# Kernel optimization log

Measured on AMD Instinct MI355X. Metric: run time of the kernel, lower is better.

The kernel has to match this reference:

```python
import jax, jax.numpy as jnp
import numpy as np

N_NODES = 50000
N_EDGES = 800000
IN_FEAT = 128
HIDDEN = 256
NUM_LAYERS = 4
NUM_CLASSES = 10
NUM_GRAPHS = 128
BN_EPS = 1e-5


def setup_inputs() -> dict:
    key = jax.random.key(0)
    ks = jax.random.split(key, 8)
    x = jax.random.normal(ks[0], (N_NODES, IN_FEAT), dtype=jnp.float32)
    edge_index = jax.random.randint(ks[1], (2, N_EDGES), 0, N_NODES, dtype=jnp.int64)
    batch = jax.random.randint(ks[2], (N_NODES,), 0, NUM_GRAPHS, dtype=jnp.int64)
    W1 = jax.random.normal(ks[3], (IN_FEAT, HIDDEN), dtype=jnp.float32) * 0.05
    b1 = jnp.zeros((HIDDEN,), jnp.float32)
    gamma = jnp.ones((HIDDEN,), jnp.float32)
    beta = jnp.zeros((HIDDEN,), jnp.float32)
    run_mean = jnp.zeros((HIDDEN,), jnp.float32)
    run_var = jnp.ones((HIDDEN,), jnp.float32)
    Ws = jax.random.normal(ks[4], (NUM_LAYERS - 1, HIDDEN, HIDDEN), dtype=jnp.float32) * 0.05
    bs = jnp.zeros((NUM_LAYERS - 1, HIDDEN), jnp.float32)
    W2 = jax.random.normal(ks[5], (HIDDEN, NUM_CLASSES), dtype=jnp.float32) * 0.05
    b2 = jnp.zeros((NUM_CLASSES,), jnp.float32)
    return {"x": x, "edge_index": edge_index, "batch": batch,
            "W1": W1, "b1": b1, "gamma": gamma, "beta": beta,
            "run_mean": run_mean, "run_var": run_var,
            "Ws": Ws, "bs": bs, "W2": W2, "b2": b2}


def _gcn_conv(h, W, b, src, dst, norm, n):
    # x' = D^-1/2 (A+I) D^-1/2 (x W) + b   (PyG GCNConv with self-loops)
    h = h @ W                                   # [N, out]
    msg = h[src] * norm[:, None]                # [E+N, out]
    agg = jax.ops.segment_sum(msg, dst, num_segments=n)
    return agg + b


def reference(x, edge_index, batch, W1, b1, gamma, beta, run_mean, run_var, Ws, bs, W2, b2):
    n = x.shape[0]
    loop = jnp.arange(n, dtype=edge_index.dtype)
    src = jnp.concatenate([edge_index[0], loop])
    dst = jnp.concatenate([edge_index[1], loop])
    # symmetric GCN normalization with self-loops (deg >= 1, no inf)
    deg = jax.ops.segment_sum(jnp.ones_like(dst, x.dtype), dst, num_segments=n)
    dinv = jax.lax.rsqrt(deg)
    norm = dinv[src] * dinv[dst]

    h = _gcn_conv(x, W1, b1, src, dst, norm, n)
    # BatchNorm in eval mode: running statistics
    h = (h - run_mean) * jax.lax.rsqrt(run_var + BN_EPS) * gamma + beta
    h = jax.nn.relu(h)
    for i in range(Ws.shape[0]):
        h = jax.nn.relu(_gcn_conv(h, Ws[i], bs[i], src, dst, norm, n))

    # global mean pool over graphs
    sums = jax.ops.segment_sum(h, batch, num_segments=NUM_GRAPHS)
    cnts = jax.ops.segment_sum(jnp.ones((n,), x.dtype), batch, num_segments=NUM_GRAPHS)
    pooled = sums / jnp.maximum(cnts, 1.0)[:, None]

    logits = pooled @ W2 + b2
    return jax.nn.log_softmax(logits, axis=-1)
```

## Files before the change

kernel.cpp:

```cpp
#include <hip/hip_runtime.h>
#include <math.h>

#define N_NODES 50000
#define N_EDGES 800000
#define IN_FEAT 128
#define HIDDEN 256
#define NUM_GRAPHS 128
#define NUM_CLASSES 10
#define BN_EPS 1e-5f

#define NCHUNK ((N_NODES + 255) / 256)
#define BINW 512
#define NBINS ((N_NODES + BINW - 1) / BINW)

typedef __attribute__((ext_vector_type(8))) short bf16x8;
typedef __attribute__((ext_vector_type(16))) float f32x16;
typedef __attribute__((ext_vector_type(2))) float f32x2;

__device__ __forceinline__ ushort f2bf(float f) {
    union { float f; uint u; } c; c.f = f;
    uint u = c.u;
    return (ushort)((u + 0x7FFFu + ((u >> 16) & 1u)) >> 16);
}
__device__ __forceinline__ float bf2f(ushort h) {
    union { uint u; float f; } c; c.u = ((uint)h) << 16;
    return c.f;
}
__device__ __forceinline__ unsigned char f2fp8(float f) {
    return (unsigned char)(__builtin_amdgcn_cvt_pk_fp8_f32(f, f, 0, false) & 0xFF);
}

__global__ void k_count(const int* __restrict__ dst, int* __restrict__ cnt) {
    int e = blockIdx.x * 256 + threadIdx.x;
    if (e < N_EDGES) atomicAdd(&cnt[dst[e]], 1);
}

__global__ __launch_bounds__(512) void k_count_batch(const int* __restrict__ batch,
                                                     int* __restrict__ gcnt) {
    __shared__ int hist[NUM_GRAPHS];
    int t = threadIdx.x;
    if (t < NUM_GRAPHS) hist[t] = 0;
    __syncthreads();
    int v = blockIdx.x * 512 + t;
    if (v < N_NODES) atomicAdd(&hist[batch[v]], 1);
    __syncthreads();
    if (t < NUM_GRAPHS && hist[t] > 0) atomicAdd(&gcnt[t], hist[t]);
}

__global__ __launch_bounds__(256) void k_chunksum(const int* __restrict__ cnt,
                                                  int* __restrict__ csum) {
    int i = blockIdx.x * 256 + threadIdx.x;
    int v = (i < N_NODES) ? cnt[i] : 0;
#pragma unroll
    for (int off = 32; off; off >>= 1) v += __shfl_down(v, off, 64);
    __shared__ int ws[4];
    if ((threadIdx.x & 63) == 0) ws[threadIdx.x >> 6] = v;
    __syncthreads();
    if (threadIdx.x == 0) csum[blockIdx.x] = ws[0] + ws[1] + ws[2] + ws[3];
}

__global__ __launch_bounds__(256) void k_scan2(const int* __restrict__ csum,
                                               int* __restrict__ choff,
                                               const int* __restrict__ gcnt,
                                               int* __restrict__ goff,
                                               int* __restrict__ gcur) {
    __shared__ int s[256];
    int t = threadIdx.x;
    if (blockIdx.x == 0) {
        int v = (t < NCHUNK) ? csum[t] : 0;
        s[t] = v;
        __syncthreads();
#pragma unroll
        for (int off = 1; off < 256; off <<= 1) {
            int add = (t >= off) ? s[t - off] : 0;
            __syncthreads();
            s[t] += add;
            __syncthreads();
        }
        if (t < NCHUNK) choff[t] = s[t] - v;
    } else {
        int v = (t < NUM_GRAPHS) ? gcnt[t] : 0;
        s[t] = v;
        __syncthreads();
#pragma unroll
        for (int off = 1; off < NUM_GRAPHS; off <<= 1) {
            int add = (t >= off && t < NUM_GRAPHS) ? s[t - off] : 0;
            __syncthreads();
            if (t < NUM_GRAPHS) s[t] += add;
            __syncthreads();
        }
        if (t < NUM_GRAPHS) {
            goff[t] = s[t] - v;
            gcur[t] = s[t] - v;
            if (t == NUM_GRAPHS - 1) goff[NUM_GRAPHS] = s[t];
        }
    }
}

__global__ __launch_bounds__(256) void k_apply(const int* __restrict__ cnt,
                                               const int* __restrict__ choff,
                                               int* __restrict__ rowp,
                                               float* __restrict__ dinv) {
    __shared__ int s[256];
    int t = threadIdx.x;
    int i = blockIdx.x * 256 + t;
    int c = (i < N_NODES) ? cnt[i] : 0;
    s[t] = c;
    __syncthreads();
#pragma unroll
    for (int off = 1; off < 256; off <<= 1) {
        int add = (t >= off) ? s[t - off] : 0;
        __syncthreads();
        s[t] += add;
        __syncthreads();
    }
    int incl = s[t];
    int base = choff[blockIdx.x];
    if (i < N_NODES) {
        int ex = base + incl - c;
        rowp[i] = ex;
        dinv[i] = rsqrtf(1.0f + (float)c);
        if (i == N_NODES - 1) rowp[N_NODES] = base + incl;
    }
}

__global__ void k_initbins(const int* __restrict__ rowp, int* __restrict__ bincur) {
    int b = threadIdx.x;
    if (b < NBINS) bincur[b] = rowp[b * BINW];
}

#define FILLA_EPT 8
__global__ __launch_bounds__(256) void k_binA(const int* __restrict__ src,
                                              const int* __restrict__ dst,
                                              int* __restrict__ bincur,
                                              uint* __restrict__ pairs) {
    __shared__ int hist[NBINS];
    __shared__ int base[NBINS];
    int t = threadIdx.x;
    for (int i = t; i < NBINS; i += 256) hist[i] = 0;
    __syncthreads();
    int e0 = blockIdx.x * (256 * FILLA_EPT);
    int mybin[FILLA_EPT], myoff[FILLA_EPT];
    uint mypair[FILLA_EPT];
#pragma unroll
    for (int j = 0; j < FILLA_EPT; ++j) {
        int e = e0 + j * 256 + t;
        mybin[j] = -1;
        if (e < N_EDGES) {
            int d = dst[e], s = src[e];
            int b = d >> 9;
            mybin[j] = b;
            mypair[j] = (uint)s | ((uint)(d & (BINW - 1)) << 16);
            myoff[j] = atomicAdd(&hist[b], 1);
        }
    }
    __syncthreads();
    for (int i = t; i < NBINS; i += 256)
        base[i] = atomicAdd(&bincur[i], hist[i]);
    __syncthreads();
#pragma unroll
    for (int j = 0; j < FILLA_EPT; ++j) {
        if (mybin[j] >= 0) pairs[base[mybin[j]] + myoff[j]] = mypair[j];
    }
}

__global__ __launch_bounds__(512) void k_binB(const uint* __restrict__ pairs,
                                              const int* __restrict__ rowp,
                                              int* __restrict__ col) {
    __shared__ int cur[BINW];
    int b = blockIdx.x;
    int v0 = b * BINW;
    int t = threadIdx.x;
    int vend = min(v0 + BINW, N_NODES);
    for (int i = t; i < vend - v0; i += 512) cur[i] = rowp[v0 + i];
    __syncthreads();
    int lo = rowp[v0];
    int hi = rowp[vend];
    for (int i = lo + t; i < hi; i += 512) {
        uint pr = pairs[i];
        int dl = pr >> 16;
        int s = pr & 0xFFFF;
        int slot = atomicAdd(&cur[dl], 1);
        col[slot] = s;
    }
}

__global__ __launch_bounds__(512) void k_fillg(const int* __restrict__ batch,
                                               int* __restrict__ gcur,
                                               int* __restrict__ nlist) {
    __shared__ int hist[NUM_GRAPHS];
    __shared__ int base[NUM_GRAPHS];
    int t = threadIdx.x;
    if (t < NUM_GRAPHS) hist[t] = 0;
    __syncthreads();
    int v = blockIdx.x * 512 + t;
    int g = -1, off = 0;
    if (v < N_NODES) {
        g = batch[v];
        off = atomicAdd(&hist[g], 1);
    }
    __syncthreads();
    if (t < NUM_GRAPHS) base[t] = atomicAdd(&gcur[t], hist[t]);
    __syncthreads();
    if (g >= 0) nlist[base[g] + off] = v;
}

__global__ void k_prescale(const float* __restrict__ x, const float* __restrict__ dinv,
                           unsigned char* __restrict__ p0) {
    int i = blockIdx.x * 256 + threadIdx.x;
    if (i < N_NODES * IN_FEAT / 4) {
        float4 v = ((const float4*)x)[i];
        float d = dinv[i / (IN_FEAT / 4)];
        uchar4 o;
        o.x = f2fp8(v.x * d); o.y = f2fp8(v.y * d);
        o.z = f2fp8(v.z * d); o.w = f2fp8(v.w * d);
        ((uchar4*)p0)[i] = o;
    }
}

__global__ __launch_bounds__(256) void k_agg128(const unsigned char* __restrict__ p,
                                                const int* __restrict__ col,
                                                const int* __restrict__ row_ptr,
                                                const float* __restrict__ dinv,
                                                ushort* __restrict__ out) {
    const int F = IN_FEAT;
    int wave = threadIdx.x >> 6;
    int lane = threadIdx.x & 63;
    int v = blockIdx.x * 4 + wave;
    if (v >= N_NODES) return;
    int rp0 = row_ptr[v], rp1 = row_ptr[v + 1];
    float d = dinv[v];
    ushort um = ((const ushort*)(p + (size_t)v * F))[lane];
    f32x2 m = __builtin_amdgcn_cvt_pk_f32_fp8((int)um, false);
    float a0 = m.x, a1 = m.y;
    int i = rp0;
    for (; i + 8 <= rp1; i += 8) {
        int s0 = col[i],     s1 = col[i + 1], s2 = col[i + 2], s3 = col[i + 3];
        int s4 = col[i + 4], s5 = col[i + 5], s6 = col[i + 6], s7 = col[i + 7];
        ushort u0 = ((const ushort*)(p + (size_t)s0 * F))[lane];
        ushort u1 = ((const ushort*)(p + (size_t)s1 * F))[lane];
        ushort u2 = ((const ushort*)(p + (size_t)s2 * F))[lane];
        ushort u3 = ((const ushort*)(p + (size_t)s3 * F))[lane];
        ushort u4 = ((const ushort*)(p + (size_t)s4 * F))[lane];
        ushort u5 = ((const ushort*)(p + (size_t)s5 * F))[lane];
        ushort u6 = ((const ushort*)(p + (size_t)s6 * F))[lane];
        ushort u7 = ((const ushort*)(p + (size_t)s7 * F))[lane];
        f32x2 d0 = __builtin_amdgcn_cvt_pk_f32_fp8((int)u0, false);
        f32x2 d1 = __builtin_amdgcn_cvt_pk_f32_fp8((int)u1, false);
        f32x2 d2 = __builtin_amdgcn_cvt_pk_f32_fp8((int)u2, false);
        f32x2 d3 = __builtin_amdgcn_cvt_pk_f32_fp8((int)u3, false);
        f32x2 d4 = __builtin_amdgcn_cvt_pk_f32_fp8((int)u4, false);
        f32x2 d5 = __builtin_amdgcn_cvt_pk_f32_fp8((int)u5, false);
        f32x2 d6 = __builtin_amdgcn_cvt_pk_f32_fp8((int)u6, false);
        f32x2 d7 = __builtin_amdgcn_cvt_pk_f32_fp8((int)u7, false);
        a0 += d0.x + d1.x + d2.x + d3.x + d4.x + d5.x + d6.x + d7.x;
        a1 += d0.y + d1.y + d2.y + d3.y + d4.y + d5.y + d6.y + d7.y;
    }
    for (; i < rp1; ++i) {
        int s = col[i];
        ushort u = ((const ushort*)(p + (size_t)s * F))[lane];
        f32x2 dv = __builtin_amdgcn_cvt_pk_f32_fp8((int)u, false);
        a0 += dv.x; a1 += dv.y;
    }
    ushort2 o;
    o.x = f2bf(a0 * d); o.y = f2bf(a1 * d);
    ((ushort2*)(out + (size_t)v * F))[lane] = o;
}

__global__ __launch_bounds__(256) void k_agg8(const unsigned char* __restrict__ p,
                                              const int* __restrict__ col,
                                              const int* __restrict__ row_ptr,
                                              const float* __restrict__ dinv,
                                              ushort* __restrict__ out) {
    const int F = HIDDEN;
    int wave = threadIdx.x >> 6;
    int lane = threadIdx.x & 63;
    int v = blockIdx.x * 4 + wave;
    if (v >= N_NODES) return;
    int rp0 = row_ptr[v], rp1 = row_ptr[v + 1];
    float d = dinv[v];
    uint um = ((const uint*)(p + (size_t)v * F))[lane];
    f32x2 mlo = __builtin_amdgcn_cvt_pk_f32_fp8((int)um, false);
    f32x2 mhi = __builtin_amdgcn_cvt_pk_f32_fp8((int)um, true);
    float a0 = mlo.x, a1 = mlo.y, a2 = mhi.x, a3 = mhi.y;
    int i = rp0;
    for (; i + 8 <= rp1; i += 8) {
        int s0 = col[i],     s1 = col[i + 1], s2 = col[i + 2], s3 = col[i + 3];
        int s4 = col[i + 4], s5 = col[i + 5], s6 = col[i + 6], s7 = col[i + 7];
        uint u0 = ((const uint*)(p + (size_t)s0 * F))[lane];
        uint u1 = ((const uint*)(p + (size_t)s1 * F))[lane];
        uint u2 = ((const uint*)(p + (size_t)s2 * F))[lane];
        uint u3 = ((const uint*)(p + (size_t)s3 * F))[lane];
        uint u4 = ((const uint*)(p + (size_t)s4 * F))[lane];
        uint u5 = ((const uint*)(p + (size_t)s5 * F))[lane];
        uint u6 = ((const uint*)(p + (size_t)s6 * F))[lane];
        uint u7 = ((const uint*)(p + (size_t)s7 * F))[lane];
#pragma unroll
        for (int j = 0; j < 8; ++j) {
            uint u = (j == 0) ? u0 : (j == 1) ? u1 : (j == 2) ? u2 : (j == 3) ? u3
                   : (j == 4) ? u4 : (j == 5) ? u5 : (j == 6) ? u6 : u7;
            f32x2 lo = __builtin_amdgcn_cvt_pk_f32_fp8((int)u, false);
            f32x2 hi = __builtin_amdgcn_cvt_pk_f32_fp8((int)u, true);
            a0 += lo.x; a1 += lo.y; a2 += hi.x; a3 += hi.y;
        }
    }
    for (; i < rp1; ++i) {
        int s = col[i];
        uint u = ((const uint*)(p + (size_t)s * F))[lane];
        f32x2 lo = __builtin_amdgcn_cvt_pk_f32_fp8((int)u, false);
        f32x2 hi = __builtin_amdgcn_cvt_pk_f32_fp8((int)u, true);
        a0 += lo.x; a1 += lo.y; a2 += hi.x; a3 += hi.y;
    }
    ushort4 o;
    o.x = f2bf(a0 * d); o.y = f2bf(a1 * d); o.z = f2bf(a2 * d); o.w = f2bf(a3 * d);
    ((ushort4*)(out + (size_t)v * F))[lane] = o;
}

__device__ __forceinline__ void repack_one(const float* W, ushort* Wp, int KT, int tid) {
    int lane = tid & 63;
    int kt = (tid >> 6) % KT;
    int nt = (tid >> 6) / KT;
    int n = nt * 32 + (lane & 31);
    int kb = kt * 16 + (lane >> 5) * 8;
    ushort o[8];
#pragma unroll
    for (int j = 0; j < 8; ++j) o[j] = f2bf(W[(size_t)(kb + j) * HIDDEN + n]);
    ushort4* dst = (ushort4*)(Wp + (size_t)tid * 8);
    dst[0] = make_ushort4(o[0], o[1], o[2], o[3]);
    dst[1] = make_ushort4(o[4], o[5], o[6], o[7]);
}

__global__ __launch_bounds__(256) void k_repackAll(const float* __restrict__ W1,
                                                   const float* __restrict__ Wsp,
                                                   ushort* __restrict__ Wp1,
                                                   ushort* __restrict__ Wp2,
                                                   ushort* __restrict__ Wp3,
                                                   ushort* __restrict__ Wp4) {
    const int N1 = 8 * 8 * 64;
    const int NH = 8 * 16 * 64;
    int tid = blockIdx.x * 256 + threadIdx.x;
    if (tid < N1) repack_one(W1, Wp1, 8, tid);
    else if (tid < N1 + NH) repack_one(Wsp + 0 * HIDDEN * HIDDEN, Wp2, 16, tid - N1);
    else if (tid < N1 + 2 * NH) repack_one(Wsp + 1 * HIDDEN * HIDDEN, Wp3, 16, tid - N1 - NH);
    else if (tid < N1 + 3 * NH) repack_one(Wsp + 2 * HIDDEN * HIDDEN, Wp4, 16, tid - N1 - 2 * NH);
}

template <int KDIM, int EPI>
__global__ __launch_bounds__(256) void k_mgemm(const ushort* __restrict__ A,
                                               const ushort* __restrict__ Wp,
                                               const float* __restrict__ bias,
                                               const float* __restrict__ gamma,
                                               const float* __restrict__ beta,
                                               const float* __restrict__ mean,
                                               const float* __restrict__ var,
                                               const float* __restrict__ dinv,
                                               unsigned char* __restrict__ out) {
    constexpr int KT = KDIM / 16;
    int t = threadIdx.x;
    int wv = t >> 6, lane = t & 63;
    int rg = wv >> 1;
    int ch = wv & 1;
    int row0 = blockIdx.x * 64 + rg * 32;
    int nt0 = ch * 4;
    int r32 = lane & 31, hh = lane >> 5;
    int arow = row0 + r32;
    if (arow >= N_NODES) arow = N_NODES - 1;

    f32x16 acc[4];
#pragma unroll
    for (int j = 0; j < 4; ++j)
#pragma unroll
        for (int r = 0; r < 16; ++r) acc[j][r] = 0.f;

    const ushort* aptr = A + (size_t)arow * KDIM + hh * 8;
#pragma unroll
    for (int kt = 0; kt < KT; ++kt) {
        bf16x8 af = *(const bf16x8*)(aptr + kt * 16);
#pragma unroll
        for (int j = 0; j < 4; ++j) {
            bf16x8 bfv = *(const bf16x8*)(Wp + ((size_t)((nt0 + j) * KT + kt) * 64 + lane) * 8);
            acc[j] = __builtin_amdgcn_mfma_f32_32x32x16_bf16(af, bfv, acc[j], 0, 0, 0);
        }
    }

    int rowb = row0 + 4 * hh;
    float bi[4], sc[4], sh[4];
#pragma unroll
    for (int j = 0; j < 4; ++j) {
        int colc = (nt0 + j) * 32 + r32;
        bi[j] = bias[colc];
        if constexpr (EPI == 0) {
            float s = gamma[colc] * rsqrtf(var[colc] + BN_EPS);
            sc[j] = s; sh[j] = beta[colc] - mean[colc] * s;
        }
    }
#pragma unroll
    for (int r = 0; r < 16; ++r) {
        int grow = rowb + (r & 3) + 8 * (r >> 2);
        if (grow < N_NODES) {
            float d = (EPI == 2) ? 1.f : dinv[grow];
#pragma unroll
            for (int j = 0; j < 4; ++j) {
                float y = acc[j][r] + bi[j];
                if constexpr (EPI == 0) y = y * sc[j] + sh[j];
                y = fmaxf(y, 0.f);
                y *= d;
                out[(size_t)grow * HIDDEN + (nt0 + j) * 32 + r32] = f2fp8(y);
            }
        }
    }
}

__global__ __launch_bounds__(256) void k_pool2(const unsigned char* __restrict__ h,
                                               const int* __restrict__ nlist,
                                               const int* __restrict__ goff,
                                               float* __restrict__ sums) {
    int bid = blockIdx.x;
    int chunk = bid & 3;
    int half = (bid >> 2) & 1;
    int g = bid >> 3;
    int lo = goff[g], hi = goff[g + 1];
    int w = threadIdx.x >> 6, l = threadIdx.x & 63;
    const unsigned char* hp = h + half * 128 + l * 2;
    float a0 = 0.f, a1 = 0.f;
    int i = lo + chunk * 4 + w;
    for (; i + 48 < hi; i += 64) {
        int v0 = nlist[i], v1 = nlist[i + 16], v2 = nlist[i + 32], v3 = nlist[i + 48];
        uchar2 q0 = *(const uchar2*)(hp + (size_t)v0 * HIDDEN);
        uchar2 q1 = *(const uchar2*)(hp + (size_t)v1 * HIDDEN);
        uchar2 q2 = *(const uchar2*)(hp + (size_t)v2 * HIDDEN);
        uchar2 q3 = *(const uchar2*)(hp + (size_t)v3 * HIDDEN);
        f32x2 d0 = __builtin_amdgcn_cvt_pk_f32_fp8((int)(q0.x | (q0.y << 8)), false);
        f32x2 d1 = __builtin_amdgcn_cvt_pk_f32_fp8((int)(q1.x | (q1.y << 8)), false);
        f32x2 d2 = __builtin_amdgcn_cvt_pk_f32_fp8((int)(q2.x | (q2.y << 8)), false);
        f32x2 d3 = __builtin_amdgcn_cvt_pk_f32_fp8((int)(q3.x | (q3.y << 8)), false);
        a0 += d0.x + d1.x + d2.x + d3.x;
        a1 += d0.y + d1.y + d2.y + d3.y;
    }
    for (; i < hi; i += 16) {
        int v = nlist[i];
        uchar2 q = *(const uchar2*)(hp + (size_t)v * HIDDEN);
        f32x2 dv = __builtin_amdgcn_cvt_pk_f32_fp8((int)(q.x | (q.y << 8)), false);
        a0 += dv.x; a1 += dv.y;
    }
    __shared__ float red[4][128];
    red[w][l * 2] = a0;
    red[w][l * 2 + 1] = a1;
    __syncthreads();
    int t = threadIdx.x;
    if (t < 128) {
        float s = red[0][t] + red[1][t] + red[2][t] + red[3][t];
        atomicAdd(&sums[(size_t)g * HIDDEN + half * 128 + t], s);
    }
}

__global__ __launch_bounds__(256) void k_logits(const float* __restrict__ sums,
                                                const int* __restrict__ gcnt,
                                                const float* __restrict__ W2,
                                                const float* __restrict__ b2,
                                                float* __restrict__ outp) {
    __shared__ float pooled[HIDDEN];
    int g = blockIdx.x;
    int t = threadIdx.x;
    float inv = 1.0f / fmaxf((float)gcnt[g], 1.0f);
    pooled[t] = sums[(size_t)g * HIDDEN + t] * inv;
    __syncthreads();
    if (t < 64) {
        float lg = -INFINITY;
        if (t < NUM_CLASSES) {
            lg = b2[t];
            for (int k = 0; k < HIDDEN; ++k) lg += pooled[k] * W2[k * NUM_CLASSES + t];
        }
        float m = lg;
        for (int off = 1; off < 16; off <<= 1) m = fmaxf(m, __shfl_xor(m, off));
        float e = (t < 16) ? expf(lg - m) : 0.f;
        float ssum = e;
        for (int off = 1; off < 16; off <<= 1) ssum += __shfl_xor(ssum, off);
        if (t < NUM_CLASSES) outp[g * NUM_CLASSES + t] = lg - m - logf(ssum);
    }
}

extern "C" void kernel_launch(void* const* d_in, const int* in_sizes, int n_in,
                              void* d_out, int out_size, void* d_ws, size_t ws_size,
                              hipStream_t stream) {
    const float* x     = (const float*)d_in[0];
    const int*   ei    = (const int*)d_in[1];
    const int*   batch = (const int*)d_in[2];
    const float* W1    = (const float*)d_in[3];
    const float* b1    = (const float*)d_in[4];
    const float* gamma = (const float*)d_in[5];
    const float* beta  = (const float*)d_in[6];
    const float* rmean = (const float*)d_in[7];
    const float* rvar  = (const float*)d_in[8];
    const float* Wsp   = (const float*)d_in[9];
    const float* bsp   = (const float*)d_in[10];
    const float* W2    = (const float*)d_in[11];
    const float* b2    = (const float*)d_in[12];
    float* out = (float*)d_out;

    char* w = (char*)d_ws;
    size_t off = 0;
    auto alloc = [&](size_t bytes) -> void* {
        void* p = w + off;
        off = (off + bytes + 255) & ~(size_t)255;
        return p;
    };
    int*    cnt    = (int*)alloc((size_t)N_NODES * 4);
    int*    gcnt   = (int*)alloc((size_t)NUM_GRAPHS * 4);
    int*    rowp   = (int*)alloc((size_t)(N_NODES + 1) * 4);
    int*    bincur = (int*)alloc((size_t)NBINS * 4);
    uint*   pairs  = (uint*)alloc((size_t)N_EDGES * 4);
    int*    col    = (int*)alloc((size_t)N_EDGES * 4);
    float*  dinv   = (float*)alloc((size_t)N_NODES * 4);
    int*    csum   = (int*)alloc((size_t)NCHUNK * 4);
    int*    choff  = (int*)alloc((size_t)NCHUNK * 4);
    int*    goff   = (int*)alloc((size_t)(NUM_GRAPHS + 1) * 4);
    int*    gcur   = (int*)alloc((size_t)NUM_GRAPHS * 4);
    int*    nlist  = (int*)alloc((size_t)N_NODES * 4);
    float*  sums   = (float*)alloc((size_t)NUM_GRAPHS * HIDDEN * 4);
    ushort* Wp1    = (ushort*)alloc((size_t)8 * 8 * 64 * 8 * 2);
    ushort* Wp2    = (ushort*)alloc((size_t)8 * 16 * 64 * 8 * 2);
    ushort* Wp3    = (ushort*)alloc((size_t)8 * 16 * 64 * 8 * 2);
    ushort* Wp4    = (ushort*)alloc((size_t)8 * 16 * 64 * 8 * 2);
    ushort* bufB   = (ushort*)alloc((size_t)N_NODES * HIDDEN * 2);
    unsigned char* p8 = (unsigned char*)alloc((size_t)N_NODES * IN_FEAT);
    unsigned char* h8 = (unsigned char*)alloc((size_t)N_NODES * HIDDEN);

    hipMemsetAsync(cnt, 0, (size_t)N_NODES * 4, stream);
    hipMemsetAsync(gcnt, 0, (size_t)NUM_GRAPHS * 4, stream);
    hipMemsetAsync(sums, 0, (size_t)NUM_GRAPHS * HIDDEN * 4, stream);

    const int* srcp = ei;
    const int* dstp = ei + N_EDGES;

    k_count<<<(N_EDGES + 255) / 256, 256, 0, stream>>>(dstp, cnt);
    k_count_batch<<<(N_NODES + 511) / 512, 512, 0, stream>>>(batch, gcnt);
    k_chunksum<<<NCHUNK, 256, 0, stream>>>(cnt, csum);
    k_scan2<<<2, 256, 0, stream>>>(csum, choff, gcnt, goff, gcur);
    k_apply<<<NCHUNK, 256, 0, stream>>>(cnt, choff, rowp, dinv);
    k_initbins<<<1, 128, 0, stream>>>(rowp, bincur);
    k_binA<<<(N_EDGES + 256 * FILLA_EPT - 1) / (256 * FILLA_EPT), 256, 0, stream>>>(
        srcp, dstp, bincur, pairs);
    k_binB<<<NBINS, 512, 0, stream>>>(pairs, rowp, col);
    k_fillg<<<(N_NODES + 511) / 512, 512, 0, stream>>>(batch, gcur, nlist);

    k_repackAll<<<(8 * 8 * 64 + 3 * 8 * 16 * 64 + 255) / 256, 256, 0, stream>>>(
        W1, Wsp, Wp1, Wp2, Wp3, Wp4);

    const int GG = (N_NODES + 63) / 64;
    const int NB4 = (N_NODES + 3) / 4;

    k_prescale<<<(N_NODES * IN_FEAT / 4 + 255) / 256, 256, 0, stream>>>(x, dinv, p8);
    k_agg128<<<NB4, 256, 0, stream>>>(p8, col, rowp, dinv, bufB);
    k_mgemm<IN_FEAT, 0><<<GG, 256, 0, stream>>>(bufB, Wp1, b1, gamma, beta, rmean, rvar, dinv, h8);

    k_agg8<<<NB4, 256, 0, stream>>>(h8, col, rowp, dinv, bufB);
    k_mgemm<HIDDEN, 1><<<GG, 256, 0, stream>>>(bufB, Wp2, bsp + 0 * HIDDEN,
                                               nullptr, nullptr, nullptr, nullptr, dinv, h8);

    k_agg8<<<NB4, 256, 0, stream>>>(h8, col, rowp, dinv, bufB);
    k_mgemm<HIDDEN, 1><<<GG, 256, 0, stream>>>(bufB, Wp3, bsp + 1 * HIDDEN,
                                               nullptr, nullptr, nullptr, nullptr, dinv, h8);

    k_agg8<<<NB4, 256, 0, stream>>>(h8, col, rowp, dinv, bufB);
    k_mgemm<HIDDEN, 2><<<GG, 256, 0, stream>>>(bufB, Wp4, bsp + 2 * HIDDEN,
                                               nullptr, nullptr, nullptr, nullptr, dinv, h8);

    k_pool2<<<NUM_GRAPHS * 2 * 4, 256, 0, stream>>>(h8, nlist, goff, sums);
    k_logits<<<NUM_GRAPHS, 256, 0, stream>>>(sums, gcnt, W2, b2, out);
}
```

Before: 358.3 us.

## Switch aggregated activations and weights to fp8 and use fp8 MFMA GEMMs

The aggregation kernels now write their output as fp8 instead of bf16, the weights are repacked to fp8, and the dense GEMMs use the 32x32x16 fp8 MFMA instead of the bf16 one. This halves the intermediate activation traffic between each aggregation and its GEMM and doubles MFMA throughput, at the cost of more quantization error in both operands. Separately, the bin-cursor initialisation is folded into k_apply, which removes one tiny kernel launch.

```diff
diff --git a/kernel.cpp b/kernel.cpp
--- a/kernel.cpp
+++ b/kernel.cpp
@@ -13,7 +13,6 @@
 #define BINW 512
 #define NBINS ((N_NODES + BINW - 1) / BINW)
 
-typedef __attribute__((ext_vector_type(8))) short bf16x8;
 typedef __attribute__((ext_vector_type(16))) float f32x16;
 typedef __attribute__((ext_vector_type(2))) float f32x2;
 
@@ -100,7 +99,8 @@
 __global__ __launch_bounds__(256) void k_apply(const int* __restrict__ cnt,
                                                const int* __restrict__ choff,
                                                int* __restrict__ rowp,
-                                               float* __restrict__ dinv) {
+                                               float* __restrict__ dinv,
+                                               int* __restrict__ bincur) {
     __shared__ int s[256];
     int t = threadIdx.x;
     int i = blockIdx.x * 256 + t;
@@ -120,13 +120,9 @@
         int ex = base + incl - c;
         rowp[i] = ex;
         dinv[i] = rsqrtf(1.0f + (float)c);
+        if ((i & (BINW - 1)) == 0) bincur[i / BINW] = ex;
         if (i == N_NODES - 1) rowp[N_NODES] = base + incl;
     }
-}
-
-__global__ void k_initbins(const int* __restrict__ rowp, int* __restrict__ bincur) {
-    int b = threadIdx.x;
-    if (b < NBINS) bincur[b] = rowp[b * BINW];
 }
 
 #define FILLA_EPT 8
@@ -222,7 +218,7 @@
                                                 const int* __restrict__ col,
                                                 const int* __restrict__ row_ptr,
                                                 const float* __restrict__ dinv,
-                                                ushort* __restrict__ out) {
+                                                unsigned char* __restrict__ out) {
     const int F = IN_FEAT;
     int wave = threadIdx.x >> 6;
     int lane = threadIdx.x & 63;
@@ -262,16 +258,16 @@
         f32x2 dv = __builtin_amdgcn_cvt_pk_f32_fp8((int)u, false);
         a0 += dv.x; a1 += dv.y;
     }
-    ushort2 o;
-    o.x = f2bf(a0 * d); o.y = f2bf(a1 * d);
-    ((ushort2*)(out + (size_t)v * F))[lane] = o;
+    uchar2 o;
+    o.x = f2fp8(a0 * d); o.y = f2fp8(a1 * d);
+    ((uchar2*)(out + (size_t)v * F))[lane] = o;
 }
 
 __global__ __launch_bounds__(256) void k_agg8(const unsigned char* __restrict__ p,
                                               const int* __restrict__ col,
                                               const int* __restrict__ row_ptr,
                                               const float* __restrict__ dinv,
-                                              ushort* __restrict__ out) {
+                                              unsigned char* __restrict__ out) {
     const int F = HIDDEN;
     int wave = threadIdx.x >> 6;
     int lane = threadIdx.x & 63;
@@ -311,31 +307,36 @@
         f32x2 hi = __builtin_amdgcn_cvt_pk_f32_fp8((int)u, true);
         a0 += lo.x; a1 += lo.y; a2 += hi.x; a3 += hi.y;
     }
-    ushort4 o;
-    o.x = f2bf(a0 * d); o.y = f2bf(a1 * d); o.z = f2bf(a2 * d); o.w = f2bf(a3 * d);
-    ((ushort4*)(out + (size_t)v * F))[lane] = o;
-}
-
-__device__ __forceinline__ void repack_one(const float* W, ushort* Wp, int KT, int tid) {
+    uchar4 o;
+    o.x = f2fp8(a0 * d); o.y = f2fp8(a1 * d); o.z = f2fp8(a2 * d); o.w = f2fp8(a3 * d);
+    ((uchar4*)(out + (size_t)v * F))[lane] = o;
+}
+
+__device__ __forceinline__ void repack_one(const float* W, unsigned char* Wp, int KT, int tid) {
     int lane = tid & 63;
     int kt = (tid >> 6) % KT;
     int nt = (tid >> 6) / KT;
     int n = nt * 32 + (lane & 31);
     int kb = kt * 16 + (lane >> 5) * 8;
-    ushort o[8];
-#pragma unroll
-    for (int j = 0; j < 8; ++j) o[j] = f2bf(W[(size_t)(kb + j) * HIDDEN + n]);
-    ushort4* dst = (ushort4*)(Wp + (size_t)tid * 8);
-    dst[0] = make_ushort4(o[0], o[1], o[2], o[3]);
-    dst[1] = make_ushort4(o[4], o[5], o[6], o[7]);
+    uchar4 lo, hi;
+    lo.x = f2fp8(W[(size_t)(kb + 0) * HIDDEN + n]);
+    lo.y = f2fp8(W[(size_t)(kb + 1) * HIDDEN + n]);
+    lo.z = f2fp8(W[(size_t)(kb + 2) * HIDDEN + n]);
+    lo.w = f2fp8(W[(size_t)(kb + 3) * HIDDEN + n]);
+    hi.x = f2fp8(W[(size_t)(kb + 4) * HIDDEN + n]);
+    hi.y = f2fp8(W[(size_t)(kb + 5) * HIDDEN + n]);
+    hi.z = f2fp8(W[(size_t)(kb + 6) * HIDDEN + n]);
+    hi.w = f2fp8(W[(size_t)(kb + 7) * HIDDEN + n]);
+    ((uchar4*)(Wp + (size_t)tid * 8))[0] = lo;
+    ((uchar4*)(Wp + (size_t)tid * 8))[1] = hi;
 }
 
 __global__ __launch_bounds__(256) void k_repackAll(const float* __restrict__ W1,
                                                    const float* __restrict__ Wsp,
-                                                   ushort* __restrict__ Wp1,
-                                                   ushort* __restrict__ Wp2,
-                                                   ushort* __restrict__ Wp3,
-                                                   ushort* __restrict__ Wp4) {
+                                                   unsigned char* __restrict__ Wp1,
+                                                   unsigned char* __restrict__ Wp2,
+                                                   unsigned char* __restrict__ Wp3,
+                                                   unsigned char* __restrict__ Wp4) {
     const int N1 = 8 * 8 * 64;
     const int NH = 8 * 16 * 64;
     int tid = blockIdx.x * 256 + threadIdx.x;
@@ -346,8 +347,8 @@
 }
 
 template <int KDIM, int EPI>
-__global__ __launch_bounds__(256) void k_mgemm(const ushort* __restrict__ A,
-                                               const ushort* __restrict__ Wp,
+__global__ __launch_bounds__(256) void k_mgemm(const unsigned char* __restrict__ A,
+                                               const unsigned char* __restrict__ Wp,
                                                const float* __restrict__ bias,
                                                const float* __restrict__ gamma,
                                                const float* __restrict__ beta,
@@ -372,14 +373,14 @@
 #pragma unroll
         for (int r = 0; r < 16; ++r) acc[j][r] = 0.f;
 
-    const ushort* aptr = A + (size_t)arow * KDIM + hh * 8;
+    const unsigned char* aptr = A + (size_t)arow * KDIM + hh * 8;
 #pragma unroll
     for (int kt = 0; kt < KT; ++kt) {
-        bf16x8 af = *(const bf16x8*)(aptr + kt * 16);
+        long av = *(const long*)(aptr + kt * 16);
 #pragma unroll
         for (int j = 0; j < 4; ++j) {
-            bf16x8 bfv = *(const bf16x8*)(Wp + ((size_t)((nt0 + j) * KT + kt) * 64 + lane) * 8);
-            acc[j] = __builtin_amdgcn_mfma_f32_32x32x16_bf16(af, bfv, acc[j], 0, 0, 0);
+            long bv = *(const long*)(Wp + ((size_t)((nt0 + j) * KT + kt) * 64 + lane) * 8);
+            acc[j] = __builtin_amdgcn_mfma_f32_32x32x16_fp8_fp8(av, bv, acc[j], 0, 0, 0);
         }
     }
 
@@ -518,13 +519,13 @@
     int*    gcur   = (int*)alloc((size_t)NUM_GRAPHS * 4);
     int*    nlist  = (int*)alloc((size_t)N_NODES * 4);
     float*  sums   = (float*)alloc((size_t)NUM_GRAPHS * HIDDEN * 4);
-    ushort* Wp1    = (ushort*)alloc((size_t)8 * 8 * 64 * 8 * 2);
-    ushort* Wp2    = (ushort*)alloc((size_t)8 * 16 * 64 * 8 * 2);
-    ushort* Wp3    = (ushort*)alloc((size_t)8 * 16 * 64 * 8 * 2);
-    ushort* Wp4    = (ushort*)alloc((size_t)8 * 16 * 64 * 8 * 2);
-    ushort* bufB   = (ushort*)alloc((size_t)N_NODES * HIDDEN * 2);
-    unsigned char* p8 = (unsigned char*)alloc((size_t)N_NODES * IN_FEAT);
-    unsigned char* h8 = (unsigned char*)alloc((size_t)N_NODES * HIDDEN);
+    unsigned char* Wp1 = (unsigned char*)alloc((size_t)8 * 8 * 64 * 8);
+    unsigned char* Wp2 = (unsigned char*)alloc((size_t)8 * 16 * 64 * 8);
+    unsigned char* Wp3 = (unsigned char*)alloc((size_t)8 * 16 * 64 * 8);
+    unsigned char* Wp4 = (unsigned char*)alloc((size_t)8 * 16 * 64 * 8);
+    unsigned char* a8  = (unsigned char*)alloc((size_t)N_NODES * HIDDEN);
+    unsigned char* p8  = (unsigned char*)alloc((size_t)N_NODES * IN_FEAT);
+    unsigned char* h8  = (unsigned char*)alloc((size_t)N_NODES * HIDDEN);
 
     hipMemsetAsync(cnt, 0, (size_t)N_NODES * 4, stream);
     hipMemsetAsync(gcnt, 0, (size_t)NUM_GRAPHS * 4, stream);
@@ -537,8 +538,7 @@
     k_count_batch<<<(N_NODES + 511) / 512, 512, 0, stream>>>(batch, gcnt);
     k_chunksum<<<NCHUNK, 256, 0, stream>>>(cnt, csum);
     k_scan2<<<2, 256, 0, stream>>>(csum, choff, gcnt, goff, gcur);
-    k_apply<<<NCHUNK, 256, 0, stream>>>(cnt, choff, rowp, dinv);
-    k_initbins<<<1, 128, 0, stream>>>(rowp, bincur);
+    k_apply<<<NCHUNK, 256, 0, stream>>>(cnt, choff, rowp, dinv, bincur);
     k_binA<<<(N_EDGES + 256 * FILLA_EPT - 1) / (256 * FILLA_EPT), 256, 0, stream>>>(
         srcp, dstp, bincur, pairs);
     k_binB<<<NBINS, 512, 0, stream>>>(pairs, rowp, col);
@@ -551,19 +551,19 @@
     const int NB4 = (N_NODES + 3) / 4;
 
     k_prescale<<<(N_NODES * IN_FEAT / 4 + 255) / 256, 256, 0, stream>>>(x, dinv, p8);
-    k_agg128<<<NB4, 256, 0, stream>>>(p8, col, rowp, dinv, bufB);
-    k_mgemm<IN_FEAT, 0><<<GG, 256, 0, stream>>>(bufB, Wp1, b1, gamma, beta, rmean, rvar, dinv, h8);
-
-    k_agg8<<<NB4, 256, 0, stream>>>(h8, col, rowp, dinv, bufB);
-    k_mgemm<HIDDEN, 1><<<GG, 256, 0, stream>>>(bufB, Wp2, bsp + 0 * HIDDEN,
+    k_agg128<<<NB4, 256, 0, stream>>>(p8, col, rowp, dinv, a8);
+    k_mgemm<IN_FEAT, 0><<<GG, 256, 0, stream>>>(a8, Wp1, b1, gamma, beta, rmean, rvar, dinv, h8);
+
+    k_agg8<<<NB4, 256, 0, stream>>>(h8, col, rowp, dinv, a8);
+    k_mgemm<HIDDEN, 1><<<GG, 256, 0, stream>>>(a8, Wp2, bsp + 0 * HIDDEN,
                                                nullptr, nullptr, nullptr, nullptr, dinv, h8);
 
-    k_agg8<<<NB4, 256, 0, stream>>>(h8, col, rowp, dinv, bufB);
-    k_mgemm<HIDDEN, 1><<<GG, 256, 0, stream>>>(bufB, Wp3, bsp + 1 * HIDDEN,
+    k_agg8<<<NB4, 256, 0, stream>>>(h8, col, rowp, dinv, a8);
+    k_mgemm<HIDDEN, 1><<<GG, 256, 0, stream>>>(a8, Wp3, bsp + 1 * HIDDEN,
                                                nullptr, nullptr, nullptr, nullptr, dinv, h8);
 
-    k_agg8<<<NB4, 256, 0, stream>>>(h8, col, rowp, dinv, bufB);
-    k_mgemm<HIDDEN, 2><<<GG, 256, 0, stream>>>(bufB, Wp4, bsp + 2 * HIDDEN,
+    k_agg8<<<NB4, 256, 0, stream>>>(h8, col, rowp, dinv, a8);
+    k_mgemm<HIDDEN, 2><<<GG, 256, 0, stream>>>(a8, Wp4, bsp + 2 * HIDDEN,
                                                nullptr, nullptr, nullptr, nullptr, dinv, h8);
 
     k_pool2<<<NUM_GRAPHS * 2 * 4, 256, 0, stream>>>(h8, nlist, goff, sums);
```

Measured after the change: 359.0 us. No clear change (+0.2%).
